# Performance work log

Measured on AMD Instinct MI355X. Metric: run time of the kernel, lower is better.

Reference implementation:

```python
import jax, jax.numpy as jnp
import numpy as np

H, W = 512, 512
N, C, J = 10000, 8, 16
T = 32  # per-gaussian raster window (pixels), stands in for the tile-sorted variable-radius kernel
INV255 = 1.0 / 255.0


def setup_inputs() -> dict:
    key = jax.random.key(0)
    ks = jax.random.split(key, 8)
    return {
        "alpha_logits": jax.random.normal(ks[0], (N, C), dtype=jnp.float32),
        "w_proj": jax.random.normal(ks[1], (N, C, J), dtype=jnp.float32),
        "psi_weights": jax.random.normal(ks[2], (N, C, J), dtype=jnp.float32),
        "xyz": jnp.tanh(jax.random.normal(ks[3], (N, 2), dtype=jnp.float32)),
        "cholesky": jax.random.uniform(ks[4], (N, 3), dtype=jnp.float32),
        "opacity": jnp.ones((N, 1), dtype=jnp.float32),
        "cluster_means": 0.5 + 0.1 * jax.random.normal(ks[5], (C, 3), dtype=jnp.float32),
        "cluster_bases": 0.1 * jax.random.normal(ks[6], (C, J, 2), dtype=jnp.float32),
    }


def _project(xyz, cholesky):
    # project_gaussians_2d: map [-1,1] means to pixel coords, build conic = inv(L L^T)
    px = 0.5 * W * (xyz[:, 0] + 1.0)
    py = 0.5 * H * (xyz[:, 1] + 1.0)
    l = cholesky + jnp.array([0.5, 0.0, 0.5], dtype=cholesky.dtype)  # PD bound as in GaussianImage
    c00 = l[:, 0] * l[:, 0]
    c01 = l[:, 0] * l[:, 1]
    c11 = l[:, 1] * l[:, 1] + l[:, 2] * l[:, 2]
    det = c00 * c11 - c01 * c01
    conic = jnp.stack([c11 / det, -c01 / det, c00 / det], axis=-1)  # [N,3]
    return jnp.stack([px, py], axis=-1), conic


def reference(alpha_logits, w_proj, psi_weights, xyz, cholesky, opacity,
              cluster_means, cluster_bases):
    alpha = jax.nn.softmax(alpha_logits, axis=1)                               # [N,C]
    soft_color = alpha @ cluster_means                                         # [N,3]
    # get_soft_features detail part: sum_c alpha[:,c] * (w[:,c] @ V_c)
    detail = jnp.einsum('nc,ncl,cld->nd', alpha, w_proj, cluster_bases)        # [N,2]
    # get_gaussian_feature_basis: sum_{c,l} outer(alpha[:,c]*w[:,c,l], psi[:,c,l])
    d_matrix = jnp.einsum('nc,ncl,mcl->nm', alpha, w_proj, psi_weights)        # [N,N]

    xys, conic = _project(xyz, cholesky)
    base = jnp.floor(xys).astype(jnp.int32)                                    # [N,2]
    offs = jnp.arange(T, dtype=jnp.int32) - T // 2
    xi = base[:, 0:1] + offs[None, :]                                          # [N,T]
    yi = base[:, 1:2] + offs[None, :]                                          # [N,T]
    dx = xys[:, 0:1] - (xi.astype(xys.dtype) + 0.5)                            # [N,T]
    dy = xys[:, 1:2] - (yi.astype(xys.dtype) + 0.5)                            # [N,T]
    sigma = (0.5 * (conic[:, 0, None, None] * dx[:, None, :] ** 2
                    + conic[:, 2, None, None] * dy[:, :, None] ** 2)
             + conic[:, 1, None, None] * dx[:, None, :] * dy[:, :, None])      # [N,Ty,Tx]
    a = jnp.minimum(0.999, opacity[:, :, None] * jnp.exp(-sigma))              # [N,Ty,Tx]
    valid = ((sigma >= 0.0) & (a > INV255)
             & (yi[:, :, None] >= 0) & (yi[:, :, None] < H)
             & (xi[:, None, :] >= 0) & (xi[:, None, :] < W))
    vals = jnp.where(valid, a, 0.0)[..., None] * soft_color[:, None, None, :]  # [N,Ty,Tx,3]
    Y = jnp.broadcast_to(yi[:, :, None], (N, T, T))
    X = jnp.broadcast_to(xi[:, None, :], (N, T, T))
    img = jnp.zeros((H, W, 3), dtype=vals.dtype).at[Y, X].add(vals, mode='drop')
    out_img = jnp.transpose(img, (2, 0, 1))                                    # [3,H,W]
    return out_img, d_matrix, detail
```

## Files before the change

### kernel.cpp

```cpp
#include <hip/hip_runtime.h>
#include <math.h>

#define N_G 10000
#define NPAD 10112
#define C_DIM 8
#define J_DIM 16
#define K_DIM 128
#define KP 128
#define H_IMG 512
#define W_IMG 512
#define HW_IMG (H_IMG*W_IMG)
#define IMG_SIZE (3*HW_IMG)
#define NTILE 79
#define NGEMM (NTILE*NTILE)

typedef unsigned short u16;
typedef _Float16 f16x8 __attribute__((ext_vector_type(8)));
typedef float f32x4 __attribute__((ext_vector_type(4)));

__device__ inline u16 f2h(float x) {
    union { _Float16 h; u16 u; } v; v.h = (_Float16)x; return v.u;
}

__global__ __launch_bounds__(256)
void prep_zero(const float* __restrict__ alog,
               const float* __restrict__ wproj,
               const float* __restrict__ psi,
               const float* __restrict__ cbases,
               u16*   __restrict__ Up,
               u16*   __restrict__ Pp,
               float* __restrict__ detail_out,
               float* __restrict__ img)
{
    const int bid = blockIdx.x;
    const int tid = threadIdx.x;

    if (bid >= 80) {
        ((float4*)img)[(size_t)(bid - 80) * 256 + tid] = make_float4(0.f,0.f,0.f,0.f);
        return;
    }

    if (bid >= 40) {
        int m = (bid - 40) * 256 + tid;
        if (m >= NPAD) return;
        u16* pr = Pp + (size_t)m * KP;
        if (m >= N_G) {
            uint4 z = make_uint4(0,0,0,0);
            uint4* p = (uint4*)pr;
            #pragma unroll
            for (int i = 0; i < 16; ++i) p[i] = z;
            return;
        }
        const float4* ps = (const float4*)(psi + (size_t)m * K_DIM);
        #pragma unroll
        for (int q = 0; q < 32; ++q) {
            float4 x = ps[q];
            uint2 hv;
            hv.x = (unsigned)f2h(x.x) | ((unsigned)f2h(x.y)<<16);
            hv.y = (unsigned)f2h(x.z) | ((unsigned)f2h(x.w)<<16);
            *(uint2*)(pr + q*4) = hv;
        }
        return;
    }

    int n = bid * 256 + tid;
    if (n >= NPAD) return;
    u16* ur = Up + (size_t)n * KP;
    if (n >= N_G) {
        uint4 z = make_uint4(0,0,0,0);
        uint4* p = (uint4*)ur;
        #pragma unroll
        for (int i = 0; i < 16; ++i) p[i] = z;
        return;
    }

    float al[C_DIM];
    const float4* ap = (const float4*)(alog + n * C_DIM);
    float4 a0 = ap[0], a1 = ap[1];
    al[0]=a0.x; al[1]=a0.y; al[2]=a0.z; al[3]=a0.w;
    al[4]=a1.x; al[5]=a1.y; al[6]=a1.z; al[7]=a1.w;
    float mx = al[0];
    #pragma unroll
    for (int c = 1; c < C_DIM; ++c) mx = fmaxf(mx, al[c]);
    float s = 0.f;
    #pragma unroll
    for (int c = 0; c < C_DIM; ++c) { al[c] = expf(al[c] - mx); s += al[c]; }
    float inv = 1.f / s;
    #pragma unroll
    for (int c = 0; c < C_DIM; ++c) al[c] *= inv;

    float d0 = 0.f, d1 = 0.f;
    const float4* wp = (const float4*)(wproj + (size_t)n * K_DIM);
    #pragma unroll
    for (int c = 0; c < C_DIM; ++c) {
        float ac = al[c];
        #pragma unroll
        for (int q = 0; q < J_DIM/4; ++q) {
            float4 w4 = wp[c*4+q];
            float4 u4;
            u4.x = ac*w4.x; u4.y = ac*w4.y; u4.z = ac*w4.z; u4.w = ac*w4.w;
            int lb = (c*J_DIM + q*4) * 2;
            d0 = fmaf(u4.x, cbases[lb+0], d0); d1 = fmaf(u4.x, cbases[lb+1], d1);
            d0 = fmaf(u4.y, cbases[lb+2], d0); d1 = fmaf(u4.y, cbases[lb+3], d1);
            d0 = fmaf(u4.z, cbases[lb+4], d0); d1 = fmaf(u4.z, cbases[lb+5], d1);
            d0 = fmaf(u4.w, cbases[lb+6], d0); d1 = fmaf(u4.w, cbases[lb+7], d1);
            uint2 hv;
            hv.x = (unsigned)f2h(u4.x) | ((unsigned)f2h(u4.y)<<16);
            hv.y = (unsigned)f2h(u4.z) | ((unsigned)f2h(u4.w)<<16);
            *(uint2*)(ur + c*J_DIM + q*4) = hv;
        }
    }
    detail_out[n*2+0] = d0;
    detail_out[n*2+1] = d1;
}

#define TILE 128

__global__ __launch_bounds__(256)
void gemm_raster(const u16* __restrict__ U, const u16* __restrict__ P,
                 const float* __restrict__ alog,
                 const float* __restrict__ xyz,
                 const float* __restrict__ chol,
                 const float* __restrict__ opac,
                 const float* __restrict__ cmeans,
                 float* __restrict__ D, float* __restrict__ img)
{
    __shared__ char smem[32768];
    char* As = smem;
    char* Bs = smem + 16384;

    const int t = threadIdx.x;
    const int w = t >> 6;
    const int l = t & 63;

    const int orig = blockIdx.x;
    const int xcd = orig & 7;
    const int lin = orig >> 3;
    const int o = (xcd == 0) ? lin : (781 + (xcd - 1) * 780 + lin);
    int row, col;
    if (o < 7 * 790) {
        const int sb = o / 790;
        const int idx = o - sb * 790;
        col = idx / 10;
        row = sb * 10 + (idx - col * 10);
    } else {
        const int idx = o - 7 * 790;
        col = idx / 9;
        row = 70 + (idx - col * 9);
    }
    const long bm = (long)row * TILE;
    const long bn = (long)col * TILE;
    const int wm = (w >> 1) * 64;
    const int wn = (w & 1) * 64;

    const char* Ub = (const char*)U;
    const char* Pb = (const char*)P;

    const int inner = ((l & 7) * 16) ^ (((l >> 3) & 7) << 4);
    const int fr  = l & 15;
    const int g   = l >> 4;
    const int fx  = g * 16;
    const int swz = (l & 7) << 4;

    f32x4 acc[4][4];
    #pragma unroll
    for (int i = 0; i < 4; ++i)
        #pragma unroll
        for (int j = 0; j < 4; ++j)
            acc[i][j] = (f32x4){0.f, 0.f, 0.f, 0.f};

    #pragma unroll
    for (int it = 0; it < 2; ++it) {
        const long kbyte = (long)it * 128;
        #pragma unroll
        for (int c = 0; c < 4; ++c) {
            const int rc = (w*4 + c)*8 + (l >> 3);
            const char* ga = Ub + (bm + rc)*256 + kbyte + inner;
            const char* gb = Pb + (bn + rc)*256 + kbyte + inner;
            __builtin_amdgcn_global_load_lds(
                (const __attribute__((address_space(1))) void*)ga,
                (__attribute__((address_space(3))) void*)(As + (w*4+c)*1024), 16, 0, 0);
            __builtin_amdgcn_global_load_lds(
                (const __attribute__((address_space(1))) void*)gb,
                (__attribute__((address_space(3))) void*)(Bs + (w*4+c)*1024), 16, 0, 0);
        }
        __syncthreads();
        #pragma unroll
        for (int kk = 0; kk < 2; ++kk) {
            f16x8 a[4], b[4];
            #pragma unroll
            for (int i = 0; i < 4; ++i) {
                const int rowa = wm + i*16 + fr;
                a[i] = *(const f16x8*)(As + rowa*128 + ((kk*64 + fx) ^ swz));
                const int rowb = wn + i*16 + fr;
                b[i] = *(const f16x8*)(Bs + rowb*128 + ((kk*64 + fx) ^ swz));
            }
            #pragma unroll
            for (int i = 0; i < 4; ++i)
                #pragma unroll
                for (int j = 0; j < 4; ++j)
                    acc[i][j] = __builtin_amdgcn_mfma_f32_16x16x32_f16(b[j], a[i], acc[i][j], 0, 0, 0);
        }
        __syncthreads();
    }

    char* wbuf = smem + w * 8192;
    const int lr4 = l >> 4;
    const int es  = l & 15;
    #pragma unroll
    for (int h = 0; h < 2; ++h) {
        #pragma unroll
        for (int ii = 0; ii < 2; ++ii) {
            const int lrow = ii*16 + fr;
            #pragma unroll
            for (int j = 0; j < 4; ++j) {
                const int ep = (j*4 + g) ^ lrow;
                *(f32x4*)(wbuf + lrow*256 + (ep & 15)*16) = acc[2*h + ii][j];
            }
        }
        asm volatile("s_waitcnt lgkmcnt(0)" ::: "memory");
        __builtin_amdgcn_sched_barrier(0);
        #pragma unroll
        for (int p = 0; p < 8; ++p) {
            const int lrow = p*4 + lr4;
            const int ep = (es ^ lrow) & 15;
            f32x4 v = *(const f32x4*)(wbuf + lrow*256 + ep*16);
            const int drow = (int)bm + wm + h*32 + lrow;
            const int dcol = (int)bn + wn + es*4;
            if (drow < N_G && dcol < N_G)
                __builtin_nontemporal_store(v, (f32x4*)(D + (size_t)drow * N_G + dcol));
        }
        asm volatile("s_waitcnt lgkmcnt(0)" ::: "memory");
        __builtin_amdgcn_sched_barrier(0);
    }

    if (orig >= 5000) return;
    #pragma unroll
    for (int g2 = 0; g2 < 2; ++g2) {
        const int n = orig * 2 + g2;
        float al[C_DIM];
        const float4* ap = (const float4*)(alog + n * C_DIM);
        float4 a0 = ap[0], a1 = ap[1];
        al[0]=a0.x; al[1]=a0.y; al[2]=a0.z; al[3]=a0.w;
        al[4]=a1.x; al[5]=a1.y; al[6]=a1.z; al[7]=a1.w;
        float mx = al[0];
        #pragma unroll
        for (int c = 1; c < C_DIM; ++c) mx = fmaxf(mx, al[c]);
        float s = 0.f;
        #pragma unroll
        for (int c = 0; c < C_DIM; ++c) { al[c] = expf(al[c] - mx); s += al[c]; }
        float inv = 1.f / s;
        float r = 0.f, gg = 0.f, b = 0.f;
        #pragma unroll
        for (int c = 0; c < C_DIM; ++c) {
            float ac = al[c] * inv;
            r  += ac * cmeans[c*3+0];
            gg += ac * cmeans[c*3+1];
            b  += ac * cmeans[c*3+2];
        }
        float px = 0.5f * W_IMG * (xyz[n*2+0] + 1.f);
        float py = 0.5f * H_IMG * (xyz[n*2+1] + 1.f);
        float l0 = chol[n*3+0] + 0.5f;
        float l1 = chol[n*3+1];
        float l2 = chol[n*3+2] + 0.5f;
        float c00 = l0*l0, c01 = l0*l1, c11 = l1*l1 + l2*l2;
        float det = c00*c11 - c01*c01;
        float idet = 1.f / det;
        float q0 = c11*idet, q1 = -c01*idet, q2 = c00*idet;
        float op = opac[n];
        int bx = (int)floorf(px);
        int by = (int)floorf(py);

        #pragma unroll
        for (int i = 0; i < 4; ++i) {
            int pix = t + i * 256;
            int tyi = pix >> 5;
            int txi = pix & 31;
            int xi = bx - 16 + txi;
            int yi = by - 16 + tyi;
            float dx = px - ((float)xi + 0.5f);
            float dy = py - ((float)yi + 0.5f);
            float sigma = 0.5f * (q0*dx*dx + q2*dy*dy) + q1*dx*dy;
            float a = fminf(0.999f, op * expf(-sigma));
            bool valid = (sigma >= 0.f) && (a > (1.0f/255.0f)) &&
                         (yi >= 0) && (yi < H_IMG) && (xi >= 0) && (xi < W_IMG);
            if (valid) {
                int idx = yi * W_IMG + xi;
                atomicAdd(img + idx,            a * r);
                atomicAdd(img + HW_IMG + idx,   a * gg);
                atomicAdd(img + 2*HW_IMG + idx, a * b);
            }
        }
    }
}

extern "C" void kernel_launch(void* const* d_in, const int* in_sizes, int n_in,
                              void* d_out, int out_size, void* d_ws, size_t ws_size,
                              hipStream_t stream) {
    const float* alog   = (const float*)d_in[0];
    const float* wproj  = (const float*)d_in[1];
    const float* psi    = (const float*)d_in[2];
    const float* xyz    = (const float*)d_in[3];
    const float* chol   = (const float*)d_in[4];
    const float* opac   = (const float*)d_in[5];
    const float* cmeans = (const float*)d_in[6];
    const float* cbases = (const float*)d_in[7];

    float* out  = (float*)d_out;
    float* img  = out;
    float* dmat = out + IMG_SIZE;
    float* det  = out + IMG_SIZE + (size_t)N_G * N_G;

    u16*   Up     = (u16*)d_ws;
    u16*   Pp     = Up + (size_t)NPAD * KP;

    prep_zero<<<848, 256, 0, stream>>>(
        alog, wproj, psi, cbases, Up, Pp, det, img);

    gemm_raster<<<NGEMM, 256, 0, stream>>>(
        Up, Pp, alog, xyz, chol, opac, cmeans, dmat, img);
}
```

Measured before the change: 104.9 us.

## Retile D GEMM to 32x512 blocks with direct global fragment loads

Replaces the 128x128 LDS-staged GEMM tile with 32-row by 512-column tiles. Each wave loads its f16 fragments straight from global memory into registers instead of staging them through LDS with global_load_lds. The epilogue is reorganised to transpose through shared memory, so each row writes 2KB contiguous spans of the output matrix. The padding grows to 10240 rows, and the block-to-XCD mapping is recomputed. The aim is wider, more coalesced stores of the large D matrix and less LDS traffic, at the cost of redundant global reads of the U rows across blocks and more padded compute.

```diff
diff --git a/kernel.cpp b/kernel.cpp
--- a/kernel.cpp
+++ b/kernel.cpp
@@ -2,17 +2,19 @@
 #include <math.h>
 
 #define N_G 10000
-#define NPAD 10112
+#define RPAD 10240
 #define C_DIM 8
 #define J_DIM 16
 #define K_DIM 128
-#define KP 128
 #define H_IMG 512
 #define W_IMG 512
 #define HW_IMG (H_IMG*W_IMG)
 #define IMG_SIZE (3*HW_IMG)
-#define NTILE 79
-#define NGEMM (NTILE*NTILE)
+#define BM 32
+#define BN 512
+#define MT 313
+#define NT 20
+#define NB_GEMM (MT*NT)
 
 typedef unsigned short u16;
 typedef _Float16 f16x8 __attribute__((ext_vector_type(8)));
@@ -42,8 +44,8 @@
 
     if (bid >= 40) {
         int m = (bid - 40) * 256 + tid;
-        if (m >= NPAD) return;
-        u16* pr = Pp + (size_t)m * KP;
+        if (m >= RPAD) return;
+        u16* pr = Pp + (size_t)m * K_DIM;
         if (m >= N_G) {
             uint4 z = make_uint4(0,0,0,0);
             uint4* p = (uint4*)pr;
@@ -64,8 +66,8 @@
     }
 
     int n = bid * 256 + tid;
-    if (n >= NPAD) return;
-    u16* ur = Up + (size_t)n * KP;
+    if (n >= RPAD) return;
+    u16* ur = Up + (size_t)n * K_DIM;
     if (n >= N_G) {
         uint4 z = make_uint4(0,0,0,0);
         uint4* p = (uint4*)ur;
@@ -114,8 +116,6 @@
     detail_out[n*2+1] = d1;
 }
 
-#define TILE 128
-
 __global__ __launch_bounds__(256)
 void gemm_raster(const u16* __restrict__ U, const u16* __restrict__ P,
                  const float* __restrict__ alog,
@@ -126,120 +126,76 @@
                  float* __restrict__ D, float* __restrict__ img)
 {
     __shared__ char smem[32768];
-    char* As = smem;
-    char* Bs = smem + 16384;
-
     const int t = threadIdx.x;
     const int w = t >> 6;
     const int l = t & 63;
+    const int fr = l & 15;
+    const int g  = l >> 4;
 
     const int orig = blockIdx.x;
     const int xcd = orig & 7;
     const int lin = orig >> 3;
-    const int o = (xcd == 0) ? lin : (781 + (xcd - 1) * 780 + lin);
-    int row, col;
-    if (o < 7 * 790) {
-        const int sb = o / 790;
-        const int idx = o - sb * 790;
-        col = idx / 10;
-        row = sb * 10 + (idx - col * 10);
-    } else {
-        const int idx = o - 7 * 790;
-        col = idx / 9;
-        row = 70 + (idx - col * 9);
-    }
-    const long bm = (long)row * TILE;
-    const long bn = (long)col * TILE;
-    const int wm = (w >> 1) * 64;
-    const int wn = (w & 1) * 64;
-
-    const char* Ub = (const char*)U;
-    const char* Pb = (const char*)P;
-
-    const int inner = ((l & 7) * 16) ^ (((l >> 3) & 7) << 4);
-    const int fr  = l & 15;
-    const int g   = l >> 4;
-    const int fx  = g * 16;
-    const int swz = (l & 7) << 4;
-
-    f32x4 acc[4][4];
-    #pragma unroll
-    for (int i = 0; i < 4; ++i)
-        #pragma unroll
-        for (int j = 0; j < 4; ++j)
+    const int o = (xcd < 4) ? xcd*783 + lin : 3132 + (xcd-4)*782 + lin;
+    const int m = o / NT;
+    const int n = o - m*NT;
+    const long bm = (long)m * BM;
+    const long bn = (long)n * BN;
+
+    const u16* Ua = U + (bm + fr) * K_DIM;
+    const u16* Pa = P + (bn + w*128 + fr) * K_DIM;
+
+    f32x4 acc[2][8];
+    #pragma unroll
+    for (int i = 0; i < 2; ++i)
+        #pragma unroll
+        for (int j = 0; j < 8; ++j)
             acc[i][j] = (f32x4){0.f, 0.f, 0.f, 0.f};
 
     #pragma unroll
-    for (int it = 0; it < 2; ++it) {
-        const long kbyte = (long)it * 128;
-        #pragma unroll
-        for (int c = 0; c < 4; ++c) {
-            const int rc = (w*4 + c)*8 + (l >> 3);
-            const char* ga = Ub + (bm + rc)*256 + kbyte + inner;
-            const char* gb = Pb + (bn + rc)*256 + kbyte + inner;
-            __builtin_amdgcn_global_load_lds(
-                (const __attribute__((address_space(1))) void*)ga,
-                (__attribute__((address_space(3))) void*)(As + (w*4+c)*1024), 16, 0, 0);
-            __builtin_amdgcn_global_load_lds(
-                (const __attribute__((address_space(1))) void*)gb,
-                (__attribute__((address_space(3))) void*)(Bs + (w*4+c)*1024), 16, 0, 0);
-        }
+    for (int kw = 0; kw < 4; ++kw) {
+        const int kb = kw*32 + g*8;
+        f16x8 a0 = *(const f16x8*)(Ua + kb);
+        f16x8 a1 = *(const f16x8*)(Ua + 16*K_DIM + kb);
+        f16x8 b[8];
+        #pragma unroll
+        for (int j = 0; j < 8; ++j)
+            b[j] = *(const f16x8*)(Pa + j*16*K_DIM + kb);
+        #pragma unroll
+        for (int j = 0; j < 8; ++j) {
+            acc[0][j] = __builtin_amdgcn_mfma_f32_16x16x32_f16(b[j], a0, acc[0][j], 0, 0, 0);
+            acc[1][j] = __builtin_amdgcn_mfma_f32_16x16x32_f16(b[j], a1, acc[1][j], 0, 0, 0);
+        }
+    }
+
+    float* lbuf = (float*)smem;
+    const int rrow = t >> 4;
+    #pragma unroll
+    for (int h = 0; h < 2; ++h) {
         __syncthreads();
         #pragma unroll
-        for (int kk = 0; kk < 2; ++kk) {
-            f16x8 a[4], b[4];
-            #pragma unroll
-            for (int i = 0; i < 4; ++i) {
-                const int rowa = wm + i*16 + fr;
-                a[i] = *(const f16x8*)(As + rowa*128 + ((kk*64 + fx) ^ swz));
-                const int rowb = wn + i*16 + fr;
-                b[i] = *(const f16x8*)(Bs + rowb*128 + ((kk*64 + fx) ^ swz));
-            }
-            #pragma unroll
-            for (int i = 0; i < 4; ++i)
-                #pragma unroll
-                for (int j = 0; j < 4; ++j)
-                    acc[i][j] = __builtin_amdgcn_mfma_f32_16x16x32_f16(b[j], a[i], acc[i][j], 0, 0, 0);
+        for (int j = 0; j < 8; ++j) {
+            const int sp = (w*32 + j*4 + g) ^ (fr & 7);
+            *(f32x4*)(lbuf + fr*512 + sp*4) = acc[h][j];
         }
         __syncthreads();
-    }
-
-    char* wbuf = smem + w * 8192;
-    const int lr4 = l >> 4;
-    const int es  = l & 15;
-    #pragma unroll
-    for (int h = 0; h < 2; ++h) {
-        #pragma unroll
-        for (int ii = 0; ii < 2; ++ii) {
-            const int lrow = ii*16 + fr;
-            #pragma unroll
-            for (int j = 0; j < 4; ++j) {
-                const int ep = (j*4 + g) ^ lrow;
-                *(f32x4*)(wbuf + lrow*256 + (ep & 15)*16) = acc[2*h + ii][j];
-            }
-        }
-        asm volatile("s_waitcnt lgkmcnt(0)" ::: "memory");
-        __builtin_amdgcn_sched_barrier(0);
+        const int drow = (int)bm + h*16 + rrow;
         #pragma unroll
         for (int p = 0; p < 8; ++p) {
-            const int lrow = p*4 + lr4;
-            const int ep = (es ^ lrow) & 15;
-            f32x4 v = *(const f32x4*)(wbuf + lrow*256 + ep*16);
-            const int drow = (int)bm + wm + h*32 + lrow;
-            const int dcol = (int)bn + wn + es*4;
+            const int sl = p*16 + (t & 15);
+            const int sp = sl ^ (rrow & 7);
+            f32x4 v = *(const f32x4*)(lbuf + rrow*512 + sp*4);
+            const int dcol = (int)bn + sl*4;
             if (drow < N_G && dcol < N_G)
                 __builtin_nontemporal_store(v, (f32x4*)(D + (size_t)drow * N_G + dcol));
         }
-        asm volatile("s_waitcnt lgkmcnt(0)" ::: "memory");
-        __builtin_amdgcn_sched_barrier(0);
     }
 
     if (orig >= 5000) return;
     #pragma unroll
     for (int g2 = 0; g2 < 2; ++g2) {
-        const int n = orig * 2 + g2;
+        const int nn = orig * 2 + g2;
         float al[C_DIM];
-        const float4* ap = (const float4*)(alog + n * C_DIM);
+        const float4* ap = (const float4*)(alog + nn * C_DIM);
         float4 a0 = ap[0], a1 = ap[1];
         al[0]=a0.x; al[1]=a0.y; al[2]=a0.z; al[3]=a0.w;
         al[4]=a1.x; al[5]=a1.y; al[6]=a1.z; al[7]=a1.w;
@@ -258,16 +214,16 @@
             gg += ac * cmeans[c*3+1];
             b  += ac * cmeans[c*3+2];
         }
-        float px = 0.5f * W_IMG * (xyz[n*2+0] + 1.f);
-        float py = 0.5f * H_IMG * (xyz[n*2+1] + 1.f);
-        float l0 = chol[n*3+0] + 0.5f;
-        float l1 = chol[n*3+1];
-        float l2 = chol[n*3+2] + 0.5f;
+        float px = 0.5f * W_IMG * (xyz[nn*2+0] + 1.f);
+        float py = 0.5f * H_IMG * (xyz[nn*2+1] + 1.f);
+        float l0 = chol[nn*3+0] + 0.5f;
+        float l1 = chol[nn*3+1];
+        float l2 = chol[nn*3+2] + 0.5f;
         float c00 = l0*l0, c01 = l0*l1, c11 = l1*l1 + l2*l2;
         float det = c00*c11 - c01*c01;
         float idet = 1.f / det;
         float q0 = c11*idet, q1 = -c01*idet, q2 = c00*idet;
-        float op = opac[n];
+        float op = opac[nn];
         int bx = (int)floorf(px);
         int by = (int)floorf(py);
 
@@ -312,11 +268,11 @@
     float* det  = out + IMG_SIZE + (size_t)N_G * N_G;
 
     u16*   Up     = (u16*)d_ws;
-    u16*   Pp     = Up + (size_t)NPAD * KP;
+    u16*   Pp     = Up + (size_t)RPAD * K_DIM;
 
     prep_zero<<<848, 256, 0, stream>>>(
         alog, wproj, psi, cbases, Up, Pp, det, img);
 
-    gemm_raster<<<NGEMM, 256, 0, stream>>>(
+    gemm_raster<<<NB_GEMM, 256, 0, stream>>>(
         Up, Pp, alog, xyz, chol, opac, cmeans, dmat, img);
 }
```

After: 167.4 us. 1.6x slower.
